# Kernel tuning notes

Measured on AMD Instinct MI355X. Metric: run time of the kernel, lower is better.

The kernel has to match this reference:

```python
import jax, jax.numpy as jnp
import numpy as np

ALPHA = 16.0
R = 8.0
SCALE = ALPHA / R  # scaling = alpha / r, same for every adapter


def setup_inputs() -> dict:
    key = jax.random.key(0)
    ks = jax.random.split(key, 5)
    B_, S, D = 4, 2048, 4096
    E, r = 8, 8
    x = jax.random.normal(ks[0], (B_, S, D), dtype=jnp.float32)
    W = jax.random.normal(ks[1], (D, D), dtype=jnp.float32) * (1.0 / np.sqrt(D))
    b = jax.random.normal(ks[2], (D,), dtype=jnp.float32) * 0.02
    A = jax.random.normal(ks[3], (E, r, D), dtype=jnp.float32) * (1.0 / np.sqrt(D))
    Bm = jax.random.normal(ks[4], (E, D, r), dtype=jnp.float32) * 0.02
    return {"x": x, "W": W, "b": b, "A": A, "B": Bm}


def reference(x, W, b, A, B):
    # base = F.linear(x, W, b)
    base = jnp.einsum('bsi,oi->bso', x, W) + b
    # lora_total = sum_e scale * (x @ A_e.T @ B_e.T); all experts stacked.
    # intermediate [B,S,E,r] is tiny (r=8)
    t = jnp.einsum('bsi,eri->bser', x, A)
    lora = jnp.einsum('bser,eor->bso', t, B) * SCALE
    return base + lora
```

## Files before the change

### kernel.cpp

```cpp
#include <hip/hip_runtime.h>
#include <hip/hip_bf16.h>

typedef unsigned short u16;
typedef __bf16 bf16x8 __attribute__((ext_vector_type(8)));
typedef float f32x4 __attribute__((ext_vector_type(4)));

constexpr int Mdim = 8192;
constexpr int Ndim = 4096;
constexpr int Kdim = 4096;
constexpr int ER   = 64;
constexpr float LSCALE = 2.0f;

__device__ __forceinline__ u16 f2bf(float f) {
    union { float f; unsigned u; } v; v.f = f;
    unsigned r = v.u + 0x7fffu + ((v.u >> 16) & 1u);
    return (u16)(r >> 16);
}

#define GLOAD_LDS16(g, l)                                             \
    __builtin_amdgcn_global_load_lds(                                 \
        (const __attribute__((address_space(1))) void*)(g),           \
        (__attribute__((address_space(3))) void*)(l), 16, 0, 0)

__global__ __launch_bounds__(256) void weff_kernel(
    const float* __restrict__ W, const float* __restrict__ A,
    const float* __restrict__ Bm, u16* __restrict__ Wb)
{
    __shared__ __align__(16) float sAc[ER][128];
    __shared__ __align__(16) float sBc[64][ER];

    const int t  = threadIdx.x;
    const int i0 = blockIdx.x * 128;
    const int o0 = blockIdx.y * 64;

#pragma unroll
    for (int p = 0; p < 8; ++p) {
        int lin = p * 1024 + t * 4;
        int er = lin >> 7, ci = lin & 127;
        *(float4*)&sAc[er][ci] = *(const float4*)(A + (size_t)er * Kdim + i0 + ci);
    }
    {
        int ol = t >> 2;
        int c  = (t & 3) * 16;
#pragma unroll
        for (int q = 0; q < 2; ++q) {
            int er = c + q * 8;
            int e  = er >> 3;
            const float* src = Bm + ((size_t)e * Ndim + (o0 + ol)) * 8;
            *(float4*)&sBc[ol][er]     = *(const float4*)(src);
            *(float4*)&sBc[ol][er + 4] = *(const float4*)(src + 4);
        }
    }
    __syncthreads();

    const int tx = t & 31;
    const int ty = t >> 5;
    float acc[8][4] = {};
#pragma unroll 4
    for (int er = 0; er < ER; ++er) {
        float4 a = *(const float4*)&sAc[er][tx * 4];
#pragma unroll
        for (int q = 0; q < 8; ++q) {
            float bv = sBc[q * 8 + ty][er];
            acc[q][0] += bv * a.x;
            acc[q][1] += bv * a.y;
            acc[q][2] += bv * a.z;
            acc[q][3] += bv * a.w;
        }
    }
#pragma unroll
    for (int q = 0; q < 8; ++q) {
        int o = o0 + q * 8 + ty;
        const float4 w = *(const float4*)(W + (size_t)o * Kdim + i0 + tx * 4);
        ushort4 st;
        st.x = f2bf(w.x + LSCALE * acc[q][0]);
        st.y = f2bf(w.y + LSCALE * acc[q][1]);
        st.z = f2bf(w.z + LSCALE * acc[q][2]);
        st.w = f2bf(w.w + LSCALE * acc[q][3]);
        *(ushort4*)(Wb + (size_t)o * Kdim + i0 + tx * 4) = st;
    }
}

__global__ __launch_bounds__(256) void cvt_x_kernel(
    const float* __restrict__ x, u16* __restrict__ xb)
{
    size_t i = (size_t)blockIdx.x * blockDim.x + threadIdx.x;
    const float4 v0 = *(const float4*)(x + i * 8);
    const float4 v1 = *(const float4*)(x + i * 8 + 4);
    uint4 o;
    o.x = (unsigned)f2bf(v0.x) | ((unsigned)f2bf(v0.y) << 16);
    o.y = (unsigned)f2bf(v0.z) | ((unsigned)f2bf(v0.w) << 16);
    o.z = (unsigned)f2bf(v1.x) | ((unsigned)f2bf(v1.y) << 16);
    o.w = (unsigned)f2bf(v1.z) | ((unsigned)f2bf(v1.w) << 16);
    *(uint4*)(xb + i * 8) = o;
}

constexpr int BM = 256, BN = 256, BK = 64;
constexpr int NT = Kdim / BK;

__global__ __launch_bounds__(512, 2) void gemm_bias_kernel(
    const u16* __restrict__ Xb, const u16* __restrict__ Wb,
    const float* __restrict__ bias, float* __restrict__ C)
{
    __shared__ __align__(16) u16 lds[65536];

    const int t    = threadIdx.x;
    const int lane = t & 63;
    const int wv   = t >> 6;
    const int wr   = wv >> 2;
    const int wc   = wv & 3;

    const int wg  = blockIdx.x;
    const int xcd = wg & 7, lid = wg >> 3;
    const int mt  = (xcd & 1) * 16 + (lid >> 2);
    const int ntl = (xcd >> 1) * 4 + (lid & 3);
    const int bm  = mt * BM;
    const int bn  = ntl * BN;

    u16* b0 = lds;
    u16* b1 = lds + 32768;

    const u16* gSrc[8]; int dOff[8];
#pragma unroll
    for (int i = 0; i < 8; ++i) {
        const int sub = i & 3;
        const int isB = i >> 2;
        const int c   = sub * 512 + t;
        const int row = c >> 3;
        const int scl = ((c ^ row) & 7) * 8;
        gSrc[i] = (isB ? Wb + (size_t)(bn + row) * Kdim
                       : Xb + (size_t)(bm + row) * Kdim) + scl;
        dOff[i] = isB * 16384 + c * 8;
    }

    const int fr  = lane & 15;
    const int cp0 = (((lane >> 4)    ) ^ (lane & 7)) * 8;
    const int cp1 = (((lane >> 4) + 4) ^ (lane & 7)) * 8;

    f32x4 acc[8][4];
#pragma unroll
    for (int i = 0; i < 8; ++i)
#pragma unroll
        for (int j = 0; j < 4; ++j)
            acc[i][j] = f32x4{0.f, 0.f, 0.f, 0.f};

    bf16x8 af[4][2];
    bf16x8 bfr[4][2];

#define DS_AF(BUF, MH)                                                        \
    _Pragma("unroll")                                                         \
    for (int mi = 0; mi < 4; ++mi) {                                          \
        const int rb = (wr * 128 + (MH) * 64 + mi * 16 + fr) * 64;            \
        af[mi][0] = *(const bf16x8*)&(BUF)[rb + cp0];                         \
        af[mi][1] = *(const bf16x8*)&(BUF)[rb + cp1];                         \
    }

#define DS_BF(BUF, NH)                                                        \
    _Pragma("unroll")                                                         \
    for (int nl = 0; nl < 2; ++nl) {                                          \
        const int ni = (NH) * 2 + nl;                                         \
        const int rb = 16384 + (wc * 64 + ni * 16 + fr) * 64;                 \
        bfr[ni][0] = *(const bf16x8*)&(BUF)[rb + cp0];                        \
        bfr[ni][1] = *(const bf16x8*)&(BUF)[rb + cp1];                        \
    }

#define MQ(MH, NH)                                                            \
    __builtin_amdgcn_s_setprio(1);                                            \
    _Pragma("unroll")                                                         \
    for (int mi = 0; mi < 4; ++mi)                                            \
        _Pragma("unroll")                                                     \
        for (int nl = 0; nl < 2; ++nl) {                                      \
            const int ni = (NH) * 2 + nl;                                     \
            acc[(MH)*4 + mi][ni] = __builtin_amdgcn_mfma_f32_16x16x32_bf16(   \
                af[mi][0], bfr[ni][0], acc[(MH)*4 + mi][ni], 0, 0, 0);        \
            acc[(MH)*4 + mi][ni] = __builtin_amdgcn_mfma_f32_16x16x32_bf16(   \
                af[mi][1], bfr[ni][1], acc[(MH)*4 + mi][ni], 0, 0, 0);        \
        }                                                                     \
    __builtin_amdgcn_s_setprio(0);

#define FENCE asm volatile("" ::: "memory")
#define BAR   __builtin_amdgcn_s_barrier(); FENCE

#define TILE(CUR, NXT, FIRST, LAST)                                           \
    {                                                                         \
        asm volatile("s_waitcnt vmcnt(0) lgkmcnt(0)" ::: "memory");           \
        BAR;                                                                  \
        if (!(FIRST)) { MQ(1, 0); }                                           \
        if (!(LAST)) {                                                        \
            _Pragma("unroll")                                                 \
            for (int i = 0; i < 8; ++i)                                       \
                GLOAD_LDS16(gSrc[i] + koff, (NXT) + dOff[i]);                 \
            koff += 64;                                                       \
        }                                                                     \
        DS_AF(CUR, 0);                                                        \
        DS_BF(CUR, 0);                                                        \
        MQ(0, 0);                                                             \
        DS_BF(CUR, 1);                                                        \
        MQ(0, 1);                                                             \
        DS_AF(CUR, 1);                                                        \
        MQ(1, 1);                                                             \
    }

#pragma unroll
    for (int i = 0; i < 8; ++i) GLOAD_LDS16(gSrc[i], b0 + dOff[i]);

    int koff = 64;

    TILE(b0, b1, 1, 0);
#pragma unroll 1
    for (int t2 = 0; t2 < (NT - 2) / 2; ++t2) {
        TILE(b1, b0, 0, 0);
        TILE(b0, b1, 0, 0);
    }
    TILE(b1, b0, 0, 1);
    MQ(1, 0);

#undef TILE
#undef MQ
#undef DS_BF
#undef DS_AF

#pragma unroll
    for (int ni = 0; ni < 4; ++ni) {
        const int col = bn + wc * 64 + ni * 16 + (lane & 15);
        const float bv = bias[col];
#pragma unroll
        for (int mi = 0; mi < 8; ++mi) {
            const int rbase = bm + wr * 128 + mi * 16 + (lane >> 4) * 4;
#pragma unroll
            for (int j = 0; j < 4; ++j)
                C[(size_t)(rbase + j) * Ndim + col] = acc[mi][ni][j] + bv;
        }
    }
}

__global__ __launch_bounds__(256) void naive_row_kernel(
    const float* __restrict__ x, const float* __restrict__ W,
    const float* __restrict__ bias, const float* __restrict__ A,
    const float* __restrict__ Bm, float* __restrict__ out)
{
    __shared__ float sx[Kdim];
    __shared__ float st[ER];
    const int m = blockIdx.x;
    const float* xr = x + (size_t)m * Kdim;
    for (int i = threadIdx.x; i < Kdim; i += 256) sx[i] = xr[i];
    __syncthreads();
    if (threadIdx.x < ER) {
        const float* ar = A + (size_t)threadIdx.x * Kdim;
        float s = 0.f;
        for (int i = 0; i < Kdim; ++i) s += sx[i] * ar[i];
        st[threadIdx.x] = s;
    }
    __syncthreads();
    for (int o = threadIdx.x; o < Ndim; o += 256) {
        const float* wr = W + (size_t)o * Kdim;
        float s = bias[o];
        for (int i = 0; i < Kdim; ++i) s += sx[i] * wr[i];
        float l = 0.f;
        for (int e = 0; e < 8; ++e) {
            const float* bp = Bm + ((size_t)e * Ndim + o) * 8;
            for (int r = 0; r < 8; ++r) l += st[e * 8 + r] * bp[r];
        }
        out[(size_t)m * Ndim + o] = s + LSCALE * l;
    }
}

extern "C" void kernel_launch(void* const* d_in, const int* in_sizes, int n_in,
                              void* d_out, int out_size, void* d_ws, size_t ws_size,
                              hipStream_t stream)
{
    const float* x  = (const float*)d_in[0];
    const float* W  = (const float*)d_in[1];
    const float* b  = (const float*)d_in[2];
    const float* A  = (const float*)d_in[3];
    const float* Bm = (const float*)d_in[4];
    float* out = (float*)d_out;

    const size_t xb_bytes = (size_t)Mdim * Kdim * 2;
    const size_t wb_bytes = (size_t)Ndim * Kdim * 2;

    if (ws_size >= xb_bytes + wb_bytes) {
        u16* Xb = (u16*)d_ws;
        u16* Wb = (u16*)((char*)d_ws + xb_bytes);
        cvt_x_kernel<<<(Mdim * (size_t)Kdim) / 8 / 256, 256, 0, stream>>>(x, Xb);
        weff_kernel<<<dim3(Kdim / 128, Ndim / 64), 256, 0, stream>>>(W, A, Bm, Wb);
        gemm_bias_kernel<<<dim3((Mdim / BM) * (Ndim / BN)), 512, 0, stream>>>(Xb, Wb, b, out);
    } else {
        naive_row_kernel<<<Mdim, 256, 0, stream>>>(x, W, b, A, Bm, out);
    }
}
```

Baseline: 284.7 us.

## Fuse preprocessing kernels and restructure GEMM into finer-grained staged pipeline

Merges the x-to-bf16 conversion and the effective-weight computation into one launch, interleaving one weight block after every eight conversion blocks, which saves a launch and lets both jobs share the GPU. The GEMM main loop is rewritten so half-tile loads are issued between MFMA quarters with partial vmcnt/lgkmcnt waits and extra barriers. The goal is to overlap global-to-LDS loads with compute more finely than the old wait-for-everything-per-tile scheme. The extra barriers and the tight prefetch ordering could add sync overhead or hazards.

```diff
diff --git a/kernel.cpp b/kernel.cpp
--- a/kernel.cpp
+++ b/kernel.cpp
@@ -22,22 +22,40 @@
         (const __attribute__((address_space(1))) void*)(g),           \
         (__attribute__((address_space(3))) void*)(l), 16, 0, 0)
 
-__global__ __launch_bounds__(256) void weff_kernel(
-    const float* __restrict__ W, const float* __restrict__ A,
-    const float* __restrict__ Bm, u16* __restrict__ Wb)
+__global__ __launch_bounds__(256) void fused_pre_kernel(
+    const float* __restrict__ x, const float* __restrict__ W,
+    const float* __restrict__ A, const float* __restrict__ Bm,
+    u16* __restrict__ Xb, u16* __restrict__ Wb)
 {
     __shared__ __align__(16) float sAc[ER][128];
     __shared__ __align__(16) float sBc[64][ER];
 
+    const int bx = blockIdx.x;
     const int t  = threadIdx.x;
-    const int i0 = blockIdx.x * 128;
-    const int o0 = blockIdx.y * 64;
+
+    if ((bx % 9) != 8) {
+        const int ci = (bx / 9) * 8 + (bx % 9);
+        const size_t i = ((size_t)ci * 256 + t) * 8;
+        const float4 v0 = *(const float4*)(x + i);
+        const float4 v1 = *(const float4*)(x + i + 4);
+        uint4 o;
+        o.x = (unsigned)f2bf(v0.x) | ((unsigned)f2bf(v0.y) << 16);
+        o.y = (unsigned)f2bf(v0.z) | ((unsigned)f2bf(v0.w) << 16);
+        o.z = (unsigned)f2bf(v1.x) | ((unsigned)f2bf(v1.y) << 16);
+        o.w = (unsigned)f2bf(v1.z) | ((unsigned)f2bf(v1.w) << 16);
+        *(uint4*)(Xb + i) = o;
+        return;
+    }
+
+    const int w  = bx / 9;
+    const int i0 = (w & 31) * 128;
+    const int o0 = (w >> 5) * 64;
 
 #pragma unroll
     for (int p = 0; p < 8; ++p) {
         int lin = p * 1024 + t * 4;
-        int er = lin >> 7, ci = lin & 127;
-        *(float4*)&sAc[er][ci] = *(const float4*)(A + (size_t)er * Kdim + i0 + ci);
+        int er = lin >> 7, ci2 = lin & 127;
+        *(float4*)&sAc[er][ci2] = *(const float4*)(A + (size_t)er * Kdim + i0 + ci2);
     }
     {
         int ol = t >> 2;
@@ -71,32 +89,17 @@
 #pragma unroll
     for (int q = 0; q < 8; ++q) {
         int o = o0 + q * 8 + ty;
-        const float4 w = *(const float4*)(W + (size_t)o * Kdim + i0 + tx * 4);
+        const float4 wv4 = *(const float4*)(W + (size_t)o * Kdim + i0 + tx * 4);
         ushort4 st;
-        st.x = f2bf(w.x + LSCALE * acc[q][0]);
-        st.y = f2bf(w.y + LSCALE * acc[q][1]);
-        st.z = f2bf(w.z + LSCALE * acc[q][2]);
-        st.w = f2bf(w.w + LSCALE * acc[q][3]);
+        st.x = f2bf(wv4.x + LSCALE * acc[q][0]);
+        st.y = f2bf(wv4.y + LSCALE * acc[q][1]);
+        st.z = f2bf(wv4.z + LSCALE * acc[q][2]);
+        st.w = f2bf(wv4.w + LSCALE * acc[q][3]);
         *(ushort4*)(Wb + (size_t)o * Kdim + i0 + tx * 4) = st;
     }
 }
 
-__global__ __launch_bounds__(256) void cvt_x_kernel(
-    const float* __restrict__ x, u16* __restrict__ xb)
-{
-    size_t i = (size_t)blockIdx.x * blockDim.x + threadIdx.x;
-    const float4 v0 = *(const float4*)(x + i * 8);
-    const float4 v1 = *(const float4*)(x + i * 8 + 4);
-    uint4 o;
-    o.x = (unsigned)f2bf(v0.x) | ((unsigned)f2bf(v0.y) << 16);
-    o.y = (unsigned)f2bf(v0.z) | ((unsigned)f2bf(v0.w) << 16);
-    o.z = (unsigned)f2bf(v1.x) | ((unsigned)f2bf(v1.y) << 16);
-    o.w = (unsigned)f2bf(v1.z) | ((unsigned)f2bf(v1.w) << 16);
-    *(uint4*)(xb + i * 8) = o;
-}
-
 constexpr int BM = 256, BN = 256, BK = 64;
-constexpr int NT = Kdim / BK;
 
 __global__ __launch_bounds__(512, 2) void gemm_bias_kernel(
     const u16* __restrict__ Xb, const u16* __restrict__ Wb,
@@ -117,25 +120,28 @@
     const int bm  = mt * BM;
     const int bn  = ntl * BN;
 
-    u16* b0 = lds;
-    u16* b1 = lds + 32768;
-
-    const u16* gSrc[8]; int dOff[8];
-#pragma unroll
-    for (int i = 0; i < 8; ++i) {
-        const int sub = i & 3;
-        const int isB = i >> 2;
-        const int c   = sub * 512 + t;
-        const int row = c >> 3;
-        const int scl = ((c ^ row) & 7) * 8;
-        gSrc[i] = (isB ? Wb + (size_t)(bn + row) * Kdim
-                       : Xb + (size_t)(bm + row) * Kdim) + scl;
-        dOff[i] = isB * 16384 + c * 8;
-    }
+    u16* buf0 = lds;
+    u16* buf1 = lds + 32768;
+
+    const int rl  = t >> 3;
+    const int scl = ((t ^ (t >> 3)) & 7) * 8;
+    const u16* aSrc0 = Xb + (size_t)(bm + rl) * Kdim + scl;
+    const u16* aSrc1 = Xb + (size_t)(bm + 128 + rl) * Kdim + scl;
+    const u16* bSrc0 = Wb + (size_t)(bn + rl) * Kdim + scl;
+    const u16* bSrc1 = Wb + (size_t)(bn + 128 + rl) * Kdim + scl;
+    constexpr size_t R64 = (size_t)64 * Kdim;
+
+#define STG(BUF, SLOT, SRCP, KO)                                              \
+    do {                                                                      \
+        GLOAD_LDS16((SRCP) + (KO), (BUF) + (SLOT) + t * 8);                   \
+        GLOAD_LDS16((SRCP) + (KO) + R64, (BUF) + (SLOT) + 4096 + t * 8);      \
+    } while (0)
 
     const int fr  = lane & 15;
-    const int cp0 = (((lane >> 4)    ) ^ (lane & 7)) * 8;
-    const int cp1 = (((lane >> 4) + 4) ^ (lane & 7)) * 8;
+    const int cp0 = (((lane >> 4) ^ (lane & 7)) & 7) * 8;
+    const int cp1 = ((((lane >> 4) + 4) ^ (lane & 7)) & 7) * 8;
+    const int aB  = wr * 8192;
+    const int bB  = 16384 + (wc >> 1) * 8192 + (wc & 1) * 4096;
 
     f32x4 acc[8][4];
 #pragma unroll
@@ -145,80 +151,97 @@
             acc[i][j] = f32x4{0.f, 0.f, 0.f, 0.f};
 
     bf16x8 af[4][2];
-    bf16x8 bfr[4][2];
-
-#define DS_AF(BUF, MH)                                                        \
+    bf16x8 bf0[2][2];
+    bf16x8 bf1[2][2];
+
+#define DS_A(BUF, MH)                                                         \
     _Pragma("unroll")                                                         \
     for (int mi = 0; mi < 4; ++mi) {                                          \
-        const int rb = (wr * 128 + (MH) * 64 + mi * 16 + fr) * 64;            \
+        const int rb = aB + ((MH) * 64 + mi * 16 + fr) * 64;                  \
         af[mi][0] = *(const bf16x8*)&(BUF)[rb + cp0];                         \
         af[mi][1] = *(const bf16x8*)&(BUF)[rb + cp1];                         \
     }
 
-#define DS_BF(BUF, NH)                                                        \
+#define DS_B(BUF, NH, BF)                                                     \
     _Pragma("unroll")                                                         \
-    for (int nl = 0; nl < 2; ++nl) {                                          \
-        const int ni = (NH) * 2 + nl;                                         \
-        const int rb = 16384 + (wc * 64 + ni * 16 + fr) * 64;                 \
-        bfr[ni][0] = *(const bf16x8*)&(BUF)[rb + cp0];                        \
-        bfr[ni][1] = *(const bf16x8*)&(BUF)[rb + cp1];                        \
-    }
-
-#define MQ(MH, NH)                                                            \
+    for (int ni = 0; ni < 2; ++ni) {                                          \
+        const int rb = bB + ((NH) * 32 + ni * 16 + fr) * 64;                  \
+        BF[ni][0] = *(const bf16x8*)&(BUF)[rb + cp0];                         \
+        BF[ni][1] = *(const bf16x8*)&(BUF)[rb + cp1];                         \
+    }
+
+#define MQ(MH, NH, BF)                                                        \
     __builtin_amdgcn_s_setprio(1);                                            \
     _Pragma("unroll")                                                         \
     for (int mi = 0; mi < 4; ++mi)                                            \
         _Pragma("unroll")                                                     \
-        for (int nl = 0; nl < 2; ++nl) {                                      \
-            const int ni = (NH) * 2 + nl;                                     \
-            acc[(MH)*4 + mi][ni] = __builtin_amdgcn_mfma_f32_16x16x32_bf16(   \
-                af[mi][0], bfr[ni][0], acc[(MH)*4 + mi][ni], 0, 0, 0);        \
-            acc[(MH)*4 + mi][ni] = __builtin_amdgcn_mfma_f32_16x16x32_bf16(   \
-                af[mi][1], bfr[ni][1], acc[(MH)*4 + mi][ni], 0, 0, 0);        \
+        for (int ni = 0; ni < 2; ++ni) {                                      \
+            acc[(MH)*4 + mi][(NH)*2 + ni] =                                   \
+                __builtin_amdgcn_mfma_f32_16x16x32_bf16(                      \
+                    af[mi][0], BF[ni][0], acc[(MH)*4 + mi][(NH)*2 + ni],      \
+                    0, 0, 0);                                                 \
+            acc[(MH)*4 + mi][(NH)*2 + ni] =                                   \
+                __builtin_amdgcn_mfma_f32_16x16x32_bf16(                      \
+                    af[mi][1], BF[ni][1], acc[(MH)*4 + mi][(NH)*2 + ni],      \
+                    0, 0, 0);                                                 \
         }                                                                     \
     __builtin_amdgcn_s_setprio(0);
 
 #define FENCE asm volatile("" ::: "memory")
 #define BAR   __builtin_amdgcn_s_barrier(); FENCE
-
-#define TILE(CUR, NXT, FIRST, LAST)                                           \
-    {                                                                         \
-        asm volatile("s_waitcnt vmcnt(0) lgkmcnt(0)" ::: "memory");           \
-        BAR;                                                                  \
-        if (!(FIRST)) { MQ(1, 0); }                                           \
-        if (!(LAST)) {                                                        \
-            _Pragma("unroll")                                                 \
-            for (int i = 0; i < 8; ++i)                                       \
-                GLOAD_LDS16(gSrc[i] + koff, (NXT) + dOff[i]);                 \
-            koff += 64;                                                       \
-        }                                                                     \
-        DS_AF(CUR, 0);                                                        \
-        DS_BF(CUR, 0);                                                        \
-        MQ(0, 0);                                                             \
-        DS_BF(CUR, 1);                                                        \
-        MQ(0, 1);                                                             \
-        DS_AF(CUR, 1);                                                        \
-        MQ(1, 1);                                                             \
-    }
-
-#pragma unroll
-    for (int i = 0; i < 8; ++i) GLOAD_LDS16(gSrc[i], b0 + dOff[i]);
-
-    int koff = 64;
-
-    TILE(b0, b1, 1, 0);
+#define LGKM0 asm volatile("s_waitcnt lgkmcnt(0)" ::: "memory");              \
+              __builtin_amdgcn_sched_barrier(0)
+#define VM6   asm volatile("s_waitcnt vmcnt(6)" ::: "memory")
+#define LGK8  asm volatile("s_waitcnt lgkmcnt(8)" ::: "memory")
+
+    STG(buf0, 16384, bSrc0, 0);
+    STG(buf0, 24576, bSrc1, 0);
+    STG(buf0, 0,     aSrc0, 0);
+    STG(buf0, 8192,  aSrc1, 0);
+    STG(buf1, 16384, bSrc0, 64);
+    STG(buf1, 24576, bSrc1, 64);
+    STG(buf1, 0,     aSrc0, 64);
+    VM6;
+    BAR;
+
 #pragma unroll 1
-    for (int t2 = 0; t2 < (NT - 2) / 2; ++t2) {
-        TILE(b1, b0, 0, 0);
-        TILE(b0, b1, 0, 0);
-    }
-    TILE(b1, b0, 0, 1);
-    MQ(1, 0);
-
-#undef TILE
+    for (int g = 0; g < 32; ++g) {
+        const int koO  = (2 * g + 1) * 64;
+        const int koE2 = ((2 * g + 2) & 63) * 64;
+        const int koO2 = ((2 * g + 3) & 63) * 64;
+
+        DS_A(buf0, 0); DS_B(buf0, 0, bf0);
+        STG(buf1, 8192, aSrc1, koO);
+        LGK8;
+        BAR; LGKM0; MQ(0, 0, bf0); BAR;
+        DS_B(buf0, 1, bf1);
+        STG(buf0, 16384, bSrc0, koE2);
+        BAR; LGKM0; MQ(0, 1, bf1); BAR;
+        DS_A(buf0, 1);
+        STG(buf0, 24576, bSrc1, koE2);
+        BAR; LGKM0; MQ(1, 1, bf1); BAR;
+        STG(buf0, 0, aSrc0, koE2);
+        VM6;
+        BAR; MQ(1, 0, bf0); BAR;
+        DS_A(buf1, 0); DS_B(buf1, 0, bf0);
+        STG(buf0, 8192, aSrc1, koE2);
+        LGK8;
+        BAR; LGKM0; MQ(0, 0, bf0); BAR;
+        DS_B(buf1, 1, bf1);
+        STG(buf1, 16384, bSrc0, koO2);
+        BAR; LGKM0; MQ(0, 1, bf1); BAR;
+        DS_A(buf1, 1);
+        STG(buf1, 24576, bSrc1, koO2);
+        BAR; LGKM0; MQ(1, 1, bf1); BAR;
+        STG(buf1, 0, aSrc0, koO2);
+        VM6;
+        BAR; MQ(1, 0, bf0); BAR;
+    }
+
+#undef STG
+#undef DS_A
+#undef DS_B
 #undef MQ
-#undef DS_BF
-#undef DS_AF
 
 #pragma unroll
     for (int ni = 0; ni < 4; ++ni) {
@@ -282,8 +305,7 @@
     if (ws_size >= xb_bytes + wb_bytes) {
         u16* Xb = (u16*)d_ws;
         u16* Wb = (u16*)((char*)d_ws + xb_bytes);
-        cvt_x_kernel<<<(Mdim * (size_t)Kdim) / 8 / 256, 256, 0, stream>>>(x, Xb);
-        weff_kernel<<<dim3(Kdim / 128, Ndim / 64), 256, 0, stream>>>(W, A, Bm, Wb);
+        fused_pre_kernel<<<18432, 256, 0, stream>>>(x, W, A, Bm, Xb, Wb);
         gemm_bias_kernel<<<dim3((Mdim / BM) * (Ndim / BN)), 512, 0, stream>>>(Xb, Wb, b, out);
     } else {
         naive_row_kernel<<<Mdim, 256, 0, stream>>>(x, W, b, A, Bm, out);
```

Measured after the change: 290.6 us. +2.1%, slower.
